# Kernel optimization log

Measured on AMD Instinct MI355X. Metric: run time of the kernel, lower is better.

The kernel has to match this reference:

```python
import jax, jax.numpy as jnp
import numpy as np

NUM_HEADS = 8
WINDOW = 7      # window_size -> K = 49 neighbors
DILATION = 1


def setup_inputs() -> dict:
    key = jax.random.key(0)
    k1, k2, k3 = jax.random.split(key, 3)
    shape = (4, 256, 48, 48)  # [B, C, H, W], C = num_heads * d_head
    return {
        "q": jax.random.normal(k1, shape, jnp.float32),
        "k": jax.random.normal(k2, shape, jnp.float32),
        "v": jax.random.normal(k3, shape, jnp.float32),
    }


def _neighbors(x, window, dilation):
    # x: [B, h, d, H, W] -> [B, h, K, d, H, W] via pad-and-slice shifts
    B, h, d, H, W = x.shape
    r = window // 2
    p = r * dilation
    xp = jnp.pad(x, ((0, 0), (0, 0), (0, 0), (p, p), (p, p)))
    offs = [(i - r) * dilation for i in range(window)]
    sl = [xp[:, :, :, p + dy:p + dy + H, p + dx:p + dx + W]
          for dy in offs for dx in offs]
    return jnp.stack(sl, axis=2)


def _valid_mask(H, W, window, dilation):
    # [K, H, W] boolean: True where the shifted neighbor is in-bounds
    r = window // 2
    offs = np.array([(i - r) * dilation for i in range(window)])
    hy = np.arange(H)[None, :] + offs[:, None]  # [window, H]
    wx = np.arange(W)[None, :] + offs[:, None]  # [window, W]
    vh = (hy >= 0) & (hy < H)
    vw = (wx >= 0) & (wx < W)
    mask = vh[:, None, :, None] & vw[None, :, None, :]  # [window, window, H, W]
    return jnp.asarray(mask.reshape(window * window, H, W))


def reference(q, k, v):
    B, C, H, W = q.shape
    h = NUM_HEADS
    d = C // h
    qh = q.reshape(B, h, d, H, W)
    kh = k.reshape(B, h, d, H, W)
    vh = v.reshape(B, h, d, H, W)
    kn = _neighbors(kh, WINDOW, DILATION)  # [B,h,K,d,H,W]
    vn = _neighbors(vh, WINDOW, DILATION)
    mask = _valid_mask(H, W, WINDOW, DILATION)[None, None]  # [1,1,K,H,W]
    scores = jnp.einsum('bhdxy,bhkdxy->bhkxy', qh, kn) * (d ** -0.5)
    scores = jnp.where(mask, scores, jnp.finfo(scores.dtype).min)
    attn = jax.nn.softmax(scores, axis=2)
    out = jnp.einsum('bhkxy,bhkdxy->bhdxy', attn, vn)
    return out.reshape(B, C, H, W)  # merge_heads
```

## Files before the change

### kernel.cpp

```cpp
#include <hip/hip_runtime.h>


#define H_IMG 48
#define W_IMG 48
#define DHEAD 32
#define NH    8
#define RAD   3
#define TW    16
#define TH    6
#define NPART 4
#define CPL   8
#define HALO_W  (TW + 2*RAD)
#define HALO_H  (TH + 2*RAD)
#define HALO_PX (HALO_W * HALO_H)
#define CSTR    40
#define PLANE   (H_IMG * W_IMG)
#define NTHREADS (NPART * TW * TH)

typedef _Float16 half_t;
typedef half_t half2_t __attribute__((ext_vector_type(2)));

__device__ __forceinline__ float dppadd1(float x) {
  int y = __builtin_amdgcn_update_dpp(0, __float_as_int(x), 0xB1, 0xF, 0xF, true);
  return x + __int_as_float(y);
}
__device__ __forceinline__ float dppadd2(float x) {
  int y = __builtin_amdgcn_update_dpp(0, __float_as_int(x), 0x4E, 0xF, 0xF, true);
  return x + __int_as_float(y);
}

#if defined(__has_builtin)
#if __has_builtin(__builtin_amdgcn_exp2f)
#define EXP2F(x) __builtin_amdgcn_exp2f(x)
#endif
#endif
#ifndef EXP2F
#define EXP2F(x) __expf(0.6931471805599453f * (x))
#endif

__global__ __launch_bounds__(NTHREADS, 4)
void natten_f32_kernel(const float* __restrict__ q,
                       const float* __restrict__ k,
                       const float* __restrict__ v,
                       float* __restrict__ out) {
  __shared__ __align__(16) unsigned short kl[HALO_PX * CSTR];
  __shared__ __align__(16) unsigned short vl[HALO_PX * CSTR];

  const int part = threadIdx.x;
  const int qx   = threadIdx.y;
  const int qy   = threadIdx.z;
  const int tid  = part + NPART * qx + NPART * TW * qy;
  const int x0   = blockIdx.x * TW;
  const int y0   = blockIdx.y * TH;
  const size_t cbase = (size_t)blockIdx.z * DHEAD * PLANE;

  const int gqx = x0 + qx, gqy = y0 + qy;
  const float S = 0.17677669529663687f * 1.4426950408889634f;
  const size_t qoff = cbase + (size_t)gqy * W_IMG + gqx;
  half2_t qp[4];
#pragma unroll
  for (int j = 0; j < 4; ++j) {
    qp[j].x = (half_t)(q[qoff + (size_t)(part * CPL + 2 * j) * PLANE] * S);
    qp[j].y = (half_t)(q[qoff + (size_t)(part * CPL + 2 * j + 1) * PLANE] * S);
  }

  float cmf[7];
#pragma unroll
  for (int rx = 0; rx < 7; ++rx) {
    const int gx = gqx + rx - RAD;
    cmf[rx] = ((unsigned)gx < (unsigned)W_IMG) ? 1.0f : 0.0f;
  }

  for (int i = tid; i < HALO_PX * 4; i += NTHREADS) {
    const int pix = i >> 2, chunk = i & 3;
    const int hy = pix / HALO_W;
    const int hx = pix - hy * HALO_W;
    int gy = y0 - RAD + hy;
    int gx = x0 - RAD + hx;
    gy = gy < 0 ? 0 : (gy > H_IMG - 1 ? H_IMG - 1 : gy);
    gx = gx < 0 ? 0 : (gx > W_IMG - 1 ? W_IMG - 1 : gx);
    const size_t g = cbase + (size_t)(chunk * CPL) * PLANE + (size_t)gy * W_IMG + gx;
    const float* kb = k + g;
    const float* vb = v + g;
    union { half2_t h2[4]; uint4 u; } kk, vv;
#pragma unroll
    for (int j = 0; j < 4; ++j) {
      half2_t a, b;
      a.x = (half_t)kb[(2 * j) * PLANE];  a.y = (half_t)kb[(2 * j + 1) * PLANE];
      b.x = (half_t)vb[(2 * j) * PLANE];  b.y = (half_t)vb[(2 * j + 1) * PLANE];
      kk.h2[j] = a;  vv.h2[j] = b;
    }
    *(uint4*)&kl[pix * CSTR + chunk * CPL] = kk.u;
    *(uint4*)&vl[pix * CSTR + chunk * CPL] = vv.u;
  }

  __syncthreads();

  float den = 0.0f;
  float o[CPL];
#pragma unroll
  for (int j = 0; j < CPL; ++j) o[j] = 0.0f;

  for (int ry = 0; ry < 2 * RAD + 1; ++ry) {
    const int gy = gqy + ry - RAD;
    if ((unsigned)gy >= (unsigned)H_IMG) continue;
    const int base = ((qy + ry) * HALO_W + qx) * CSTR + part * CPL;
    const unsigned short* kb = &kl[base];
    const unsigned short* vb = &vl[base];
#pragma unroll
    for (int rx = 0; rx < 7; ++rx) {
      union { uint4 u; half2_t h[4]; } kw, vw;
      kw.u = *(const uint4*)(kb + rx * CSTR);
      vw.u = *(const uint4*)(vb + rx * CSTR);
      float acc = __builtin_amdgcn_fdot2(qp[0], kw.h[0], 0.0f, false);
      acc = __builtin_amdgcn_fdot2(qp[1], kw.h[1], acc, false);
      acc = __builtin_amdgcn_fdot2(qp[2], kw.h[2], acc, false);
      acc = __builtin_amdgcn_fdot2(qp[3], kw.h[3], acc, false);
      acc = dppadd1(acc);
      acc = dppadd2(acc);
      const float p = EXP2F(acc) * cmf[rx];
      den += p;
      o[0] += p * (float)vw.h[0].x;  o[1] += p * (float)vw.h[0].y;
      o[2] += p * (float)vw.h[1].x;  o[3] += p * (float)vw.h[1].y;
      o[4] += p * (float)vw.h[2].x;  o[5] += p * (float)vw.h[2].y;
      o[6] += p * (float)vw.h[3].x;  o[7] += p * (float)vw.h[3].y;
    }
  }

  const float rden = 1.0f / den;
#pragma unroll
  for (int j = 0; j < CPL; ++j)
    out[qoff + (size_t)(part * CPL + j) * PLANE] = o[j] * rden;
}

extern "C" void kernel_launch(void* const* d_in, const int* in_sizes, int n_in,
                              void* d_out, int out_size, void* d_ws, size_t ws_size,
                              hipStream_t stream) {
  const float* q = (const float*)d_in[0];
  const float* k = (const float*)d_in[1];
  const float* v = (const float*)d_in[2];
  float* out = (float*)d_out;

  dim3 grid(W_IMG / TW, H_IMG / TH, 4 * NH);
  dim3 block(NPART, TW, TH);
  hipLaunchKernelGGL(natten_f32_kernel, grid, block, 0, stream, q, k, v, out);
}
```

Before: 101.8 us.

## Process two query rows per thread to share K/V shared-memory reads

Each thread now handles two vertically adjacent query pixels, walking 8 halo rows and reusing each loaded K/V vector for both queries where their windows overlap. This roughly halves LDS reads per output and halves the thread count per block (384 to 192 threads). The cost is more registers per thread, fewer waves for the halo load and for latency hiding, and the occupancy hint drops from 4 to 3.

```diff
diff --git a/kernel.cpp b/kernel.cpp
--- a/kernel.cpp
+++ b/kernel.cpp
@@ -8,6 +8,7 @@
 #define RAD   3
 #define TW    16
 #define TH    6
+#define NWAVE (TH / 2)
 #define NPART 4
 #define CPL   8
 #define HALO_W  (TW + 2*RAD)
@@ -15,7 +16,7 @@
 #define HALO_PX (HALO_W * HALO_H)
 #define CSTR    40
 #define PLANE   (H_IMG * W_IMG)
-#define NTHREADS (NPART * TW * TH)
+#define NTHREADS (NPART * TW * NWAVE)
 
 typedef _Float16 half_t;
 typedef half_t half2_t __attribute__((ext_vector_type(2)));
@@ -38,7 +39,50 @@
 #define EXP2F(x) __expf(0.6931471805599453f * (x))
 #endif
 
-__global__ __launch_bounds__(NTHREADS, 4)
+template<bool DA, bool DB>
+__device__ __forceinline__ void do_row(const unsigned short* kb,
+                                       const unsigned short* vb,
+                                       const half2_t* qpA, const half2_t* qpB,
+                                       const float* cmf,
+                                       float& denA, float* oA,
+                                       float& denB, float* oB) {
+#pragma unroll
+  for (int rx = 0; rx < 7; ++rx) {
+    union { uint4 u; half2_t h[4]; } kw, vw;
+    kw.u = *(const uint4*)(kb + rx * CSTR);
+    vw.u = *(const uint4*)(vb + rx * CSTR);
+    if constexpr (DA) {
+      float acc = __builtin_amdgcn_fdot2(qpA[0], kw.h[0], 0.0f, false);
+      acc = __builtin_amdgcn_fdot2(qpA[1], kw.h[1], acc, false);
+      acc = __builtin_amdgcn_fdot2(qpA[2], kw.h[2], acc, false);
+      acc = __builtin_amdgcn_fdot2(qpA[3], kw.h[3], acc, false);
+      acc = dppadd1(acc);
+      acc = dppadd2(acc);
+      const float p = EXP2F(acc) * cmf[rx];
+      denA += p;
+      oA[0] += p * (float)vw.h[0].x;  oA[1] += p * (float)vw.h[0].y;
+      oA[2] += p * (float)vw.h[1].x;  oA[3] += p * (float)vw.h[1].y;
+      oA[4] += p * (float)vw.h[2].x;  oA[5] += p * (float)vw.h[2].y;
+      oA[6] += p * (float)vw.h[3].x;  oA[7] += p * (float)vw.h[3].y;
+    }
+    if constexpr (DB) {
+      float acc = __builtin_amdgcn_fdot2(qpB[0], kw.h[0], 0.0f, false);
+      acc = __builtin_amdgcn_fdot2(qpB[1], kw.h[1], acc, false);
+      acc = __builtin_amdgcn_fdot2(qpB[2], kw.h[2], acc, false);
+      acc = __builtin_amdgcn_fdot2(qpB[3], kw.h[3], acc, false);
+      acc = dppadd1(acc);
+      acc = dppadd2(acc);
+      const float p = EXP2F(acc) * cmf[rx];
+      denB += p;
+      oB[0] += p * (float)vw.h[0].x;  oB[1] += p * (float)vw.h[0].y;
+      oB[2] += p * (float)vw.h[1].x;  oB[3] += p * (float)vw.h[1].y;
+      oB[4] += p * (float)vw.h[2].x;  oB[5] += p * (float)vw.h[2].y;
+      oB[6] += p * (float)vw.h[3].x;  oB[7] += p * (float)vw.h[3].y;
+    }
+  }
+}
+
+__global__ __launch_bounds__(NTHREADS, 3)
 void natten_f32_kernel(const float* __restrict__ q,
                        const float* __restrict__ k,
                        const float* __restrict__ v,
@@ -48,20 +92,25 @@
 
   const int part = threadIdx.x;
   const int qx   = threadIdx.y;
-  const int qy   = threadIdx.z;
-  const int tid  = part + NPART * qx + NPART * TW * qy;
+  const int wv   = threadIdx.z;
+  const int tid  = part + NPART * qx + NPART * TW * wv;
   const int x0   = blockIdx.x * TW;
   const int y0   = blockIdx.y * TH;
   const size_t cbase = (size_t)blockIdx.z * DHEAD * PLANE;
 
-  const int gqx = x0 + qx, gqy = y0 + qy;
+  const int gqx = x0 + qx;
+  const int gqyA = y0 + 2 * wv;
+  const int gqyB = gqyA + 1;
   const float S = 0.17677669529663687f * 1.4426950408889634f;
-  const size_t qoff = cbase + (size_t)gqy * W_IMG + gqx;
-  half2_t qp[4];
+  const size_t qoffA = cbase + (size_t)gqyA * W_IMG + gqx;
+  const size_t qoffB = qoffA + W_IMG;
+  half2_t qpA[4], qpB[4];
 #pragma unroll
   for (int j = 0; j < 4; ++j) {
-    qp[j].x = (half_t)(q[qoff + (size_t)(part * CPL + 2 * j) * PLANE] * S);
-    qp[j].y = (half_t)(q[qoff + (size_t)(part * CPL + 2 * j + 1) * PLANE] * S);
+    qpA[j].x = (half_t)(q[qoffA + (size_t)(part * CPL + 2 * j) * PLANE] * S);
+    qpA[j].y = (half_t)(q[qoffA + (size_t)(part * CPL + 2 * j + 1) * PLANE] * S);
+    qpB[j].x = (half_t)(q[qoffB + (size_t)(part * CPL + 2 * j) * PLANE] * S);
+    qpB[j].y = (half_t)(q[qoffB + (size_t)(part * CPL + 2 * j + 1) * PLANE] * S);
   }
 
   float cmf[7];
@@ -96,41 +145,32 @@
 
   __syncthreads();
 
-  float den = 0.0f;
-  float o[CPL];
+  float denA = 0.0f, denB = 0.0f;
+  float oA[CPL], oB[CPL];
 #pragma unroll
-  for (int j = 0; j < CPL; ++j) o[j] = 0.0f;
+  for (int j = 0; j < CPL; ++j) { oA[j] = 0.0f; oB[j] = 0.0f; }
 
-  for (int ry = 0; ry < 2 * RAD + 1; ++ry) {
-    const int gy = gqy + ry - RAD;
-    if ((unsigned)gy >= (unsigned)H_IMG) continue;
-    const int base = ((qy + ry) * HALO_W + qx) * CSTR + part * CPL;
+  for (int rr = 0; rr < 8; ++rr) {
+    const int gr = y0 + 2 * wv + rr - RAD;
+    if ((unsigned)gr >= (unsigned)H_IMG) continue;
+    const int base = ((2 * wv + rr) * HALO_W + qx) * CSTR + part * CPL;
     const unsigned short* kb = &kl[base];
     const unsigned short* vb = &vl[base];
-#pragma unroll
-    for (int rx = 0; rx < 7; ++rx) {
-      union { uint4 u; half2_t h[4]; } kw, vw;
-      kw.u = *(const uint4*)(kb + rx * CSTR);
-      vw.u = *(const uint4*)(vb + rx * CSTR);
-      float acc = __builtin_amdgcn_fdot2(qp[0], kw.h[0], 0.0f, false);
-      acc = __builtin_amdgcn_fdot2(qp[1], kw.h[1], acc, false);
-      acc = __builtin_amdgcn_fdot2(qp[2], kw.h[2], acc, false);
-      acc = __builtin_amdgcn_fdot2(qp[3], kw.h[3], acc, false);
-      acc = dppadd1(acc);
-      acc = dppadd2(acc);
-      const float p = EXP2F(acc) * cmf[rx];
-      den += p;
-      o[0] += p * (float)vw.h[0].x;  o[1] += p * (float)vw.h[0].y;
-      o[2] += p * (float)vw.h[1].x;  o[3] += p * (float)vw.h[1].y;
-      o[4] += p * (float)vw.h[2].x;  o[5] += p * (float)vw.h[2].y;
-      o[6] += p * (float)vw.h[3].x;  o[7] += p * (float)vw.h[3].y;
-    }
+    if (rr == 0)
+      do_row<true, false>(kb, vb, qpA, qpB, cmf, denA, oA, denB, oB);
+    else if (rr == 7)
+      do_row<false, true>(kb, vb, qpA, qpB, cmf, denA, oA, denB, oB);
+    else
+      do_row<true, true>(kb, vb, qpA, qpB, cmf, denA, oA, denB, oB);
   }
 
-  const float rden = 1.0f / den;
+  const float rdenA = 1.0f / denA;
+  const float rdenB = 1.0f / denB;
 #pragma unroll
-  for (int j = 0; j < CPL; ++j)
-    out[qoff + (size_t)(part * CPL + j) * PLANE] = o[j] * rden;
+  for (int j = 0; j < CPL; ++j) {
+    out[qoffA + (size_t)(part * CPL + j) * PLANE] = oA[j] * rdenA;
+    out[qoffB + (size_t)(part * CPL + j) * PLANE] = oB[j] * rdenB;
+  }
 }
 
 extern "C" void kernel_launch(void* const* d_in, const int* in_sizes, int n_in,
@@ -142,6 +182,6 @@
   float* out = (float*)d_out;
 
   dim3 grid(W_IMG / TW, H_IMG / TH, 4 * NH);
-  dim3 block(NPART, TW, TH);
+  dim3 block(NPART, TW, NWAVE);
   hipLaunchKernelGGL(natten_f32_kernel, grid, block, 0, stream, q, k, v, out);
 }
```

New measurement: 104.2 us. +2.3%, slower.

## Compute neighborhood QK and PV per row with MFMA 16x16x32 f16

Applied to the files above, without the earlier changes.

Replaces the per-thread fdot2 and DPP reduction with MFMA matrix ops. Each wave handles one query row of 16 pixels and computes scores against the 32-wide key halo row with two MFMAs, masking out-of-window keys. Probabilities are staged through shared memory as f16 and multiplied with a transposed V tile in shared memory via MFMA. The MFMAs do wasted work on the 32-key band, where only 7 of each 32 keys are valid per query, and the change adds an LDS round trip for P and a new V transpose layout. Occupancy hint drops to 3.

```diff
diff --git a/kernel.cpp b/kernel.cpp
--- a/kernel.cpp
+++ b/kernel.cpp
@@ -8,26 +8,22 @@
 #define RAD   3
 #define TW    16
 #define TH    6
-#define NPART 4
-#define CPL   8
+#define NWAVES TH
+#define NTHREADS (64 * NWAVES)
 #define HALO_W  (TW + 2*RAD)
 #define HALO_H  (TH + 2*RAD)
 #define HALO_PX (HALO_W * HALO_H)
-#define CSTR    40
+#define KL_PX   (HALO_PX + 10)
+#define KSTR    40
+#define VROW    24
+#define VSTR    (HALO_H * VROW + 8)
+#define PSTR    40
 #define PLANE   (H_IMG * W_IMG)
-#define NTHREADS (NPART * TW * TH)
 
 typedef _Float16 half_t;
-typedef half_t half2_t __attribute__((ext_vector_type(2)));
-
-__device__ __forceinline__ float dppadd1(float x) {
-  int y = __builtin_amdgcn_update_dpp(0, __float_as_int(x), 0xB1, 0xF, 0xF, true);
-  return x + __int_as_float(y);
-}
-__device__ __forceinline__ float dppadd2(float x) {
-  int y = __builtin_amdgcn_update_dpp(0, __float_as_int(x), 0x4E, 0xF, 0xF, true);
-  return x + __int_as_float(y);
-}
+typedef half_t half8_t __attribute__((ext_vector_type(8)));
+typedef __fp16 fp16x2_t __attribute__((ext_vector_type(2)));
+typedef float  f32x4  __attribute__((ext_vector_type(4)));
 
 #if defined(__has_builtin)
 #if __has_builtin(__builtin_amdgcn_exp2f)
@@ -38,38 +34,44 @@
 #define EXP2F(x) __expf(0.6931471805599453f * (x))
 #endif
 
-__global__ __launch_bounds__(NTHREADS, 4)
+__global__ __launch_bounds__(NTHREADS, 3)
 void natten_f32_kernel(const float* __restrict__ q,
                        const float* __restrict__ k,
                        const float* __restrict__ v,
                        float* __restrict__ out) {
-  __shared__ __align__(16) unsigned short kl[HALO_PX * CSTR];
-  __shared__ __align__(16) unsigned short vl[HALO_PX * CSTR];
+  __shared__ __align__(16) unsigned short kl[KL_PX * KSTR];
+  __shared__ __align__(16) unsigned short vlT[DHEAD * VSTR];
+  __shared__ __align__(16) unsigned short ps[NWAVES * 16 * PSTR];
 
-  const int part = threadIdx.x;
-  const int qx   = threadIdx.y;
-  const int qy   = threadIdx.z;
-  const int tid  = part + NPART * qx + NPART * TW * qy;
+  const int lane = threadIdx.x;
+  const int wv   = threadIdx.y;
+  const int tid  = lane + 64 * wv;
+  const int c    = lane & 15;
+  const int p    = lane >> 4;
   const int x0   = blockIdx.x * TW;
   const int y0   = blockIdx.y * TH;
   const size_t cbase = (size_t)blockIdx.z * DHEAD * PLANE;
 
-  const int gqx = x0 + qx, gqy = y0 + qy;
+  const int gqx = x0 + c;
+  const int gqy = y0 + wv;
+
   const float S = 0.17677669529663687f * 1.4426950408889634f;
   const size_t qoff = cbase + (size_t)gqy * W_IMG + gqx;
-  half2_t qp[4];
+  half8_t qf;
 #pragma unroll
-  for (int j = 0; j < 4; ++j) {
-    qp[j].x = (half_t)(q[qoff + (size_t)(part * CPL + 2 * j) * PLANE] * S);
-    qp[j].y = (half_t)(q[qoff + (size_t)(part * CPL + 2 * j + 1) * PLANE] * S);
-  }
+  for (int j = 0; j < 8; ++j)
+    qf[j] = (half_t)(q[qoff + (size_t)(p * 8 + j) * PLANE] * S);
 
-  float cmf[7];
+  float cm[2][4];
 #pragma unroll
-  for (int rx = 0; rx < 7; ++rx) {
-    const int gx = gqx + rx - RAD;
-    cmf[rx] = ((unsigned)gx < (unsigned)W_IMG) ? 1.0f : 0.0f;
-  }
+  for (int t = 0; t < 2; ++t)
+#pragma unroll
+    for (int r = 0; r < 4; ++r) {
+      const int krel = t * 16 + 4 * p + r;
+      const int gx = x0 + krel - RAD;
+      cm[t][r] = ((unsigned)(krel - c) <= 6u &&
+                  (unsigned)gx < (unsigned)W_IMG) ? 1.0f : 0.0f;
+    }
 
   for (int i = tid; i < HALO_PX * 4; i += NTHREADS) {
     const int pix = i >> 2, chunk = i & 3;
@@ -79,58 +81,94 @@
     int gx = x0 - RAD + hx;
     gy = gy < 0 ? 0 : (gy > H_IMG - 1 ? H_IMG - 1 : gy);
     gx = gx < 0 ? 0 : (gx > W_IMG - 1 ? W_IMG - 1 : gx);
-    const size_t g = cbase + (size_t)(chunk * CPL) * PLANE + (size_t)gy * W_IMG + gx;
-    const float* kb = k + g;
-    const float* vb = v + g;
-    union { half2_t h2[4]; uint4 u; } kk, vv;
+    const float* kb = k + cbase + (size_t)(chunk * 8) * PLANE + (size_t)gy * W_IMG + gx;
+    union { half_t h[8]; uint4 u; } kk;
 #pragma unroll
-    for (int j = 0; j < 4; ++j) {
-      half2_t a, b;
-      a.x = (half_t)kb[(2 * j) * PLANE];  a.y = (half_t)kb[(2 * j + 1) * PLANE];
-      b.x = (half_t)vb[(2 * j) * PLANE];  b.y = (half_t)vb[(2 * j + 1) * PLANE];
-      kk.h2[j] = a;  vv.h2[j] = b;
+    for (int j = 0; j < 8; ++j) kk.h[j] = (half_t)kb[(size_t)j * PLANE];
+    *(uint4*)&kl[pix * KSTR + chunk * 8] = kk.u;
+  }
+  if (tid < (KL_PX - HALO_PX) * (KSTR / 8)) {
+    const uint4 z = make_uint4(0, 0, 0, 0);
+    *(uint4*)&kl[HALO_PX * KSTR + tid * 8] = z;
+  }
+
+  for (int i = tid; i < DHEAD * HALO_H * 3; i += NTHREADS) {
+    const int ch = i / (HALO_H * 3);
+    const int rem = i - ch * (HALO_H * 3);
+    const int row = rem / 3, oct = rem - row * 3;
+    int gy = y0 - RAD + row;
+    gy = gy < 0 ? 0 : (gy > H_IMG - 1 ? H_IMG - 1 : gy);
+    const float* vb = v + cbase + (size_t)ch * PLANE + (size_t)gy * W_IMG;
+    union { half_t h[8]; uint4 u; } vv;
+#pragma unroll
+    for (int j = 0; j < 8; ++j) {
+      int s = oct * 8 + j;
+      int hx = s > 21 ? 21 : s;
+      int gx = x0 - RAD + hx;
+      gx = gx < 0 ? 0 : (gx > W_IMG - 1 ? W_IMG - 1 : gx);
+      vv.h[j] = (half_t)vb[gx];
     }
-    *(uint4*)&kl[pix * CSTR + chunk * CPL] = kk.u;
-    *(uint4*)&vl[pix * CSTR + chunk * CPL] = vv.u;
+    *(uint4*)&vlT[ch * VSTR + row * VROW + oct * 8] = vv.u;
+  }
+  if (tid < DHEAD) {
+    const uint4 z = make_uint4(0, 0, 0, 0);
+    *(uint4*)&vlT[tid * VSTR + HALO_H * VROW] = z;
   }
 
   __syncthreads();
 
+  f32x4 oa0 = {0.f, 0.f, 0.f, 0.f};
+  f32x4 oa1 = {0.f, 0.f, 0.f, 0.f};
+  const f32x4 z4 = {0.f, 0.f, 0.f, 0.f};
   float den = 0.0f;
-  float o[CPL];
-#pragma unroll
-  for (int j = 0; j < CPL; ++j) o[j] = 0.0f;
 
-  for (int ry = 0; ry < 2 * RAD + 1; ++ry) {
+  unsigned short* psq = &ps[(wv * 16 + c) * PSTR];
+
+  for (int ry = 0; ry < 7; ++ry) {
     const int gy = gqy + ry - RAD;
     if ((unsigned)gy >= (unsigned)H_IMG) continue;
-    const int base = ((qy + ry) * HALO_W + qx) * CSTR + part * CPL;
-    const unsigned short* kb = &kl[base];
-    const unsigned short* vb = &vl[base];
+    const int hrow = wv + ry;
+
+    union { uint4 u; half8_t h; } ka0, ka1, va0, va1, pb;
+    ka0.u = *(const uint4*)&kl[(hrow * HALO_W + c) * KSTR + p * 8];
+    ka1.u = *(const uint4*)&kl[(hrow * HALO_W + 16 + c) * KSTR + p * 8];
+    va0.u = *(const uint4*)&vlT[c * VSTR + hrow * VROW + p * 8];
+    va1.u = *(const uint4*)&vlT[(16 + c) * VSTR + hrow * VROW + p * 8];
+
+    f32x4 s0 = __builtin_amdgcn_mfma_f32_16x16x32_f16(ka0.h, qf, z4, 0, 0, 0);
+    f32x4 s1 = __builtin_amdgcn_mfma_f32_16x16x32_f16(ka1.h, qf, z4, 0, 0, 0);
+
+    float pe0[4], pe1[4];
 #pragma unroll
-    for (int rx = 0; rx < 7; ++rx) {
-      union { uint4 u; half2_t h[4]; } kw, vw;
-      kw.u = *(const uint4*)(kb + rx * CSTR);
-      vw.u = *(const uint4*)(vb + rx * CSTR);
-      float acc = __builtin_amdgcn_fdot2(qp[0], kw.h[0], 0.0f, false);
-      acc = __builtin_amdgcn_fdot2(qp[1], kw.h[1], acc, false);
-      acc = __builtin_amdgcn_fdot2(qp[2], kw.h[2], acc, false);
-      acc = __builtin_amdgcn_fdot2(qp[3], kw.h[3], acc, false);
-      acc = dppadd1(acc);
-      acc = dppadd2(acc);
-      const float p = EXP2F(acc) * cmf[rx];
-      den += p;
-      o[0] += p * (float)vw.h[0].x;  o[1] += p * (float)vw.h[0].y;
-      o[2] += p * (float)vw.h[1].x;  o[3] += p * (float)vw.h[1].y;
-      o[4] += p * (float)vw.h[2].x;  o[5] += p * (float)vw.h[2].y;
-      o[6] += p * (float)vw.h[3].x;  o[7] += p * (float)vw.h[3].y;
+    for (int r = 0; r < 4; ++r) {
+      pe0[r] = EXP2F(s0[r]) * cm[0][r];
+      pe1[r] = EXP2F(s1[r]) * cm[1][r];
+      den += pe0[r] + pe1[r];
     }
+    union { fp16x2_t h[2]; uint2 u; } w0, w1;
+    w0.h[0] = __builtin_amdgcn_cvt_pkrtz(pe0[0], pe0[1]);
+    w0.h[1] = __builtin_amdgcn_cvt_pkrtz(pe0[2], pe0[3]);
+    w1.h[0] = __builtin_amdgcn_cvt_pkrtz(pe1[0], pe1[1]);
+    w1.h[1] = __builtin_amdgcn_cvt_pkrtz(pe1[2], pe1[3]);
+    *(uint2*)((char*)psq + p * 8)      = w0.u;
+    *(uint2*)((char*)psq + 32 + p * 8) = w1.u;
+
+    pb.u = *(const uint4*)((const char*)psq + p * 16);
+
+    oa0 = __builtin_amdgcn_mfma_f32_16x16x32_f16(va0.h, pb.h, oa0, 0, 0, 0);
+    oa1 = __builtin_amdgcn_mfma_f32_16x16x32_f16(va1.h, pb.h, oa1, 0, 0, 0);
   }
 
+  den += __shfl_xor(den, 16);
+  den += __shfl_xor(den, 32);
   const float rden = 1.0f / den;
+
+  const size_t obase = cbase + (size_t)gqy * W_IMG + x0 + c;
 #pragma unroll
-  for (int j = 0; j < CPL; ++j)
-    out[qoff + (size_t)(part * CPL + j) * PLANE] = o[j] * rden;
+  for (int r = 0; r < 4; ++r) {
+    out[obase + (size_t)(4 * p + r) * PLANE]      = oa0[r] * rden;
+    out[obase + (size_t)(16 + 4 * p + r) * PLANE] = oa1[r] * rden;
+  }
 }
 
 extern "C" void kernel_launch(void* const* d_in, const int* in_sizes, int n_in,
@@ -142,6 +180,6 @@
   float* out = (float*)d_out;
 
   dim3 grid(W_IMG / TW, H_IMG / TH, 4 * NH);
-  dim3 block(NPART, TW, TH);
+  dim3 block(64, NWAVES, 1);
   hipLaunchKernelGGL(natten_f32_kernel, grid, block, 0, stream, q, k, v, out);
 }
```

Measured after the change: 96.49 us. 5.2% less time.
